# Kernel optimization log

Measured on AMD Instinct MI355X. Metric: run time of the kernel, lower is better.

Reference implementation:

```python
import jax, jax.numpy as jnp
import numpy as np
import math

B, S, D, H, F = 2, 2048, 1024, 16, 4096
DK = D // H
NEG_INF = -1000000000.0
EPS = 1e-5


def _layernorm(x, gamma, beta):
    # Faithful to source: torch.std default is unbiased (ddof=1), eps added to std
    mn = jnp.mean(x, axis=-1, keepdims=True)
    sd = jnp.std(x, axis=-1, keepdims=True, ddof=1)
    return (x - mn) / (sd + EPS) * gamma + beta


def _mha(xq, xkv, wq, bq, wk, bk, wv, bv, wo, bo, causal):
    b, sq, d = xq.shape
    sk = xkv.shape[1]
    q = (xq @ wq + bq).reshape(b, sq, H, DK).transpose(0, 2, 1, 3)   # [B,H,Sq,DK]
    k = (xkv @ wk + bk).reshape(b, sk, H, DK).transpose(0, 2, 1, 3)
    v = (xkv @ wv + bv).reshape(b, sk, H, DK).transpose(0, 2, 1, 3)
    scores = jnp.einsum('bhqd,bhkd->bhqk', q, k) / math.sqrt(DK)
    if causal:
        mask = jnp.triu(jnp.ones((sq, sk), dtype=scores.dtype), 1) * NEG_INF
        scores = scores + mask
    w = jax.nn.softmax(scores, axis=-1)
    att = jnp.einsum('bhqk,bhkd->bhqd', w, v).transpose(0, 2, 1, 3).reshape(b, sq, d)
    return att @ wo + bo


def setup_inputs() -> dict:
    key = jax.random.key(0)
    ks = jax.random.split(key, 32)
    it = iter(range(32))

    def lin(din, dout):
        kw = ks[next(it)]
        w = jax.random.normal(kw, (din, dout), jnp.float32) / math.sqrt(din)
        b = jnp.zeros((dout,), jnp.float32)
        return w, b

    X = jax.random.normal(ks[next(it)], (B, S, D), jnp.float32)
    y = jax.random.normal(ks[next(it)], (B, S, D), jnp.float32)
    wq1, bq1 = lin(D, D); wk1, bk1 = lin(D, D); wv1, bv1 = lin(D, D); wo1, bo1 = lin(D, D)
    wq2, bq2 = lin(D, D); wk2, bk2 = lin(D, D); wv2, bv2 = lin(D, D); wo2, bo2 = lin(D, D)
    wf1, bf1 = lin(D, F); wf2, bf2 = lin(F, D)
    g1 = jnp.ones((D,), jnp.float32); be1 = jnp.zeros((D,), jnp.float32)
    g2 = jnp.ones((D,), jnp.float32); be2 = jnp.zeros((D,), jnp.float32)
    g3 = jnp.ones((D,), jnp.float32); be3 = jnp.zeros((D,), jnp.float32)
    return dict(X=X, y=y,
                wq1=wq1, bq1=bq1, wk1=wk1, bk1=bk1, wv1=wv1, bv1=bv1, wo1=wo1, bo1=bo1,
                wq2=wq2, bq2=bq2, wk2=wk2, bk2=bk2, wv2=wv2, bv2=bv2, wo2=wo2, bo2=bo2,
                wf1=wf1, bf1=bf1, wf2=wf2, bf2=bf2,
                g1=g1, be1=be1, g2=g2, be2=be2, g3=g3, be3=be3)


def reference(X, y,
              wq1, bq1, wk1, bk1, wv1, bv1, wo1, bo1,
              wq2, bq2, wk2, bk2, wv2, bv2, wo2, bo2,
              wf1, bf1, wf2, bf2,
              g1, be1, g2, be2, g3, be3):
    # masked self-attention on decoder stream y (dropout = identity at inference)
    res = y
    out = _mha(y, y, wq1, bq1, wk1, bk1, wv1, bv1, wo1, bo1, causal=True)
    out = _layernorm(out + res, g1, be1)
    # cross-attention: queries from decoder, keys/values from encoder X
    res = out
    out = _mha(out, X, wq2, bq2, wk2, bk2, wv2, bv2, wo2, bo2, causal=False)
    out = _layernorm(out + res, g2, be2)
    # feed-forward (ReLU per intended semantics of the source)
    res = out
    out = jax.nn.relu(out @ wf1 + bf1) @ wf2 + bf2
    out = _layernorm(out + res, g3, be3)
    return out
```

## Files before the change

### kernel.cpp

```cpp
#include <hip/hip_runtime.h>

#define DEV __device__ __forceinline__

typedef __attribute__((ext_vector_type(8))) short short8;
typedef __attribute__((ext_vector_type(4))) float f32x4;
typedef __attribute__((ext_vector_type(4))) unsigned u32x4;

DEV unsigned short f2b(float f){
  unsigned r;
  asm("v_cvt_pk_bf16_f32 %0, %1, %1" : "=v"(r) : "v"(f));
  return (unsigned short)r;
}
DEV unsigned cvt_pk2(float lo, float hi){
  unsigned r;
  asm("v_cvt_pk_bf16_f32 %0, %1, %2" : "=v"(r) : "v"(lo), "v"(hi));
  return r;
}
DEV float b2f(unsigned short u){ unsigned v = ((unsigned)u)<<16; float f; __builtin_memcpy(&f,&v,4); return f; }

DEV void gload_lds16(const void* g, void* l){
  __builtin_amdgcn_global_load_lds((const __attribute__((address_space(1))) void*)g,
                                   (__attribute__((address_space(3))) void*)l, 16, 0, 0);
}

#define SCL 0.18033688011112042f

__global__ __launch_bounds__(256) void cvt_f32_bf16(
    const float* __restrict__ in, unsigned short* __restrict__ out, int n)
{
  int i = (blockIdx.x*256 + threadIdx.x)*4;
  if (i >= n) return;
  float4 v = *(const float4*)(in + i);
  uint2 o;
  o.x = cvt_pk2(v.x, v.y);
  o.y = cvt_pk2(v.z, v.w);
  *(uint2*)(out + i) = o;
}

struct TransAll {
  const float* W[10]; unsigned short* Wt[10];
  int K[10], N[10], swapxy[10];
};
__global__ __launch_bounds__(256) void transpose_cvt_all(TransAll p)
{
  const int z = blockIdx.z;
  const int bx = p.swapxy[z] ? blockIdx.y : blockIdx.x;
  const int by = p.swapxy[z] ? blockIdx.x : blockIdx.y;
  const int K = p.K[z], N = p.N[z];
  const int n0 = bx*32, k0 = by*32;
  if (n0 >= N || k0 >= K) return;
  const float* __restrict__ W = p.W[z];
  unsigned short* __restrict__ Wt = p.Wt[z];
  __shared__ float tile[32][33];
  int tx = threadIdx.x & 31, ty = threadIdx.x >> 5;
  #pragma unroll
  for (int j=0;j<32;j+=8)
    tile[ty+j][tx] = W[(size_t)(k0+ty+j)*N + n0+tx];
  __syncthreads();
  #pragma unroll
  for (int j=0;j<32;j+=8)
    Wt[(size_t)(n0+ty+j)*K + k0+tx] = f2b(tile[tx][ty+j]);
}

template<int EPI>
__global__ __launch_bounds__(256) void gemm_bt(
    const unsigned short* __restrict__ A,
    const unsigned short* __restrict__ Bt,
    const float* __restrict__ bias,
    unsigned short* __restrict__ C,
    int M, int N, int Kc, int LDA, int LDB)
{
  __shared__ alignas(16) unsigned short Asm_[128*32];
  __shared__ alignas(16) unsigned short Bsm_[128*32];
  const int tid = threadIdx.x;
  const int wave = tid>>6, lane = tid&63;
  const int r0 = lane&15, kq = (lane>>4)*8, cq = lane>>4;
  const int m0 = blockIdx.y*128, n0 = blockIdx.x*128;
  const int wr = wave>>1, wc = wave&1;
  const int koff = blockIdx.z * Kc;
  const bool addb = (blockIdx.z == 0);
  C += (size_t)blockIdx.z * M * N;

  f32x4 zero4 = {0.f,0.f,0.f,0.f};
  f32x4 acc[4][4];
  #pragma unroll
  for (int m=0;m<4;m++)
    #pragma unroll
    for (int n=0;n<4;n++) acc[m][n]=zero4;

  const int nk = Kc>>5;
  for (int kt=0; kt<nk; kt++){
    #pragma unroll
    for (int i=0;i<2;i++){
      int idx = i*256 + tid;
      int row = idx>>2, kc = (idx&3)<<3;
      gload_lds16(A  + (size_t)(m0+row)*LDA + koff + (kt<<5) + kc,
                  Asm_ + (size_t)(i*256 + wave*64)*8);
      gload_lds16(Bt + (size_t)(n0+row)*LDB + koff + (kt<<5) + kc,
                  Bsm_ + (size_t)(i*256 + wave*64)*8);
    }
    __syncthreads();
    short8 a[4], b[4];
    #pragma unroll
    for (int m=0;m<4;m++) a[m] = *(const short8*)&Asm_[(wr*64 + m*16 + r0)*32 + kq];
    #pragma unroll
    for (int n=0;n<4;n++) b[n] = *(const short8*)&Bsm_[(wc*64 + n*16 + r0)*32 + kq];
    #pragma unroll
    for (int m=0;m<4;m++)
      #pragma unroll
      for (int n=0;n<4;n++)
        acc[m][n] = __builtin_amdgcn_mfma_f32_16x16x32_bf16(a[m], b[n], acc[m][n], 0,0,0);
    __syncthreads();
  }

  #pragma unroll
  for (int n=0;n<4;n++){
    int col = n0 + wc*64 + n*16 + r0;
    float bs = addb ? bias[col] : 0.f;
    #pragma unroll
    for (int m=0;m<4;m++){
      int rowb = m0 + wr*64 + m*16 + cq*4;
      #pragma unroll
      for (int reg=0;reg<4;reg++){
        float v = acc[m][n][reg] + bs;
        if (EPI==1) v = fmaxf(v, 0.f);
        C[(size_t)(rowb+reg)*N + col] = f2b(v);
      }
    }
  }
}

struct QKVArgs { const unsigned short* Aw[3]; const float* bias[3]; unsigned short* out[3]; };
__global__ __launch_bounds__(256) void gemm_qkv(
    const unsigned short* __restrict__ Bt,
    QKVArgs args, int M, int K)
{
  __shared__ alignas(16) unsigned short Asm_[128*32];
  __shared__ alignas(16) unsigned short Bsm_[128*32];
  const int tid = threadIdx.x;
  const int wave = tid>>6, lane = tid&63;
  const int r0 = lane&15, kq = (lane>>4)*8, cq = lane>>4;
  const int m0 = blockIdx.y*128, n0 = blockIdx.x*128;
  const int wr = wave>>1, wc = wave&1;
  const int which = n0>>10;
  const unsigned short* __restrict__ A = args.Aw[which];

  f32x4 zero4 = {0.f,0.f,0.f,0.f};
  f32x4 acc[4][4];
  #pragma unroll
  for (int m=0;m<4;m++)
    #pragma unroll
    for (int n=0;n<4;n++) acc[m][n]=zero4;

  const int nk = K>>5;
  for (int kt=0; kt<nk; kt++){
    #pragma unroll
    for (int i=0;i<2;i++){
      int idx = i*256 + tid;
      int row = idx>>2, kc = (idx&3)<<3;
      gload_lds16(A  + (size_t)(m0+row)*K + (kt<<5) + kc,
                  Asm_ + (size_t)(i*256 + wave*64)*8);
      gload_lds16(Bt + (size_t)(n0+row)*K + (kt<<5) + kc,
                  Bsm_ + (size_t)(i*256 + wave*64)*8);
    }
    __syncthreads();
    short8 a[4], b[4];
    #pragma unroll
    for (int m=0;m<4;m++) a[m] = *(const short8*)&Asm_[(wr*64 + m*16 + r0)*32 + kq];
    #pragma unroll
    for (int n=0;n<4;n++) b[n] = *(const short8*)&Bsm_[(wc*64 + n*16 + r0)*32 + kq];
    #pragma unroll
    for (int m=0;m<4;m++)
      #pragma unroll
      for (int n=0;n<4;n++)
        acc[m][n] = __builtin_amdgcn_mfma_f32_16x16x32_bf16(a[m], b[n], acc[m][n], 0,0,0);
    __syncthreads();
  }

  const int n0l = n0 & 1023;
  unsigned short* __restrict__ Cout = args.out[which];
  const float* __restrict__ bp = args.bias[which];
  const bool isV = (which == 2);
  const float scl = (which == 0) ? SCL : 1.f;

  #pragma unroll
  for (int n=0;n<4;n++){
    int col = n0l + wc*64 + n*16 + r0;
    float bs = bp[col];
    int h_ = col>>6, dk = col&63;
    #pragma unroll
    for (int m=0;m<4;m++){
      int rowb = m0 + wr*64 + m*16 + cq*4;
      #pragma unroll
      for (int reg=0;reg<4;reg++){
        float v = (acc[m][n][reg] + bs) * scl;
        int row = rowb + reg;
        int b_ = row>>11, s_ = row&2047;
        if (isV){
          int sp = (s_ & ~31) | (((s_>>2)&3)<<3) | (((s_>>4)&1)<<2) | (s_&3);
          Cout[(((size_t)(b_*16+h_))*64 + dk)*2048 + sp] = f2b(v);
        } else {
          Cout[(((size_t)(b_*16+h_))*2048 + s_)*64 + dk] = f2b(v);
        }
      }
    }
  }
}

template<int MODE>
__global__ __launch_bounds__(256, 4) void attn_kernel(
    const unsigned short* __restrict__ Q,
    const unsigned short* __restrict__ K,
    const unsigned short* __restrict__ Vt,
    unsigned short* __restrict__ O,
    float* __restrict__ po, float* __restrict__ ml)
{
  __shared__ alignas(16) unsigned short Ksm[2][64*64];
  __shared__ alignas(16) unsigned short Vsm[2][64*64];
  const int S = 2048, DK = 64;
  const int h = blockIdx.y, b = blockIdx.z;
  const int tid = threadIdx.x, wave = tid>>6, lane = tid&63;
  const int r0 = lane&15, kq = (lane>>4)*8, cq = lane>>4;

  int qb, t0, t1, chunk = 0;
  bool partial = false;
  if (MODE==1){
    int bx = blockIdx.x;
    if (bx < 32){ qb = bx; t0 = 0; t1 = (qb<15?qb:15); chunk = 0; partial = (qb>=16); }
    else        { qb = bx-16; t0 = 16; t1 = qb; chunk = 1; partial = true; }
  } else { qb = blockIdx.x; t0 = 0; t1 = S/64 - 1; }

  const unsigned short* qh = Q  + ((size_t)(b*16+h))*S*DK;
  const unsigned short* kh = K  + ((size_t)(b*16+h))*S*DK;
  const unsigned short* vh = Vt + ((size_t)(b*16+h))*DK*S;

  const int idx0 = tid, idx1 = 256 + tid;
  const int row0 = idx0>>3, row1 = idx1>>3;
  const int cb0 = ((idx0&7) ^ (row0&7))<<3;
  const int cb1 = ((idx1&7) ^ (row1&7))<<3;
  const unsigned short* kg0 = kh + (size_t)row0*64 + cb0;
  const unsigned short* kg1 = kh + (size_t)row1*64 + cb1;
  const unsigned short* vg0 = vh + (size_t)row0*2048 + cb0;
  const unsigned short* vg1 = vh + (size_t)row1*2048 + cb1;
  const int l0 = wave*512, l1 = 2048 + wave*512;
  const int swr = (r0&7)<<3;

  short8 qa[2];
  {
    int qrow = qb*64 + wave*16 + r0;
    qa[0] = *(const short8*)&qh[(size_t)qrow*DK + kq];
    qa[1] = *(const short8*)&qh[(size_t)qrow*DK + 32 + kq];
  }
  short8 vones;
  #pragma unroll
  for (int j=0;j<8;j++) vones[j] = (short)0x3F80;

  f32x4 zero4 = {0.f,0.f,0.f,0.f};
  f32x4 o[4];
  float lr = 0.f;
  #pragma unroll
  for (int n=0;n<4;n++) o[n]=zero4;

  gload_lds16(kg0 + (size_t)t0*4096, &Ksm[0][l0]);
  gload_lds16(kg1 + (size_t)t0*4096, &Ksm[0][l1]);
  gload_lds16(vg0 + (size_t)t0*64,   &Vsm[0][l0]);
  gload_lds16(vg1 + (size_t)t0*64,   &Vsm[0][l1]);
  __syncthreads();

  int cur = 0;
  for (int t=t0; t<=t1; t++){
    if (t < t1){
      gload_lds16(kg0 + (size_t)(t+1)*4096, &Ksm[cur^1][l0]);
      gload_lds16(kg1 + (size_t)(t+1)*4096, &Ksm[cur^1][l1]);
      gload_lds16(vg0 + (size_t)(t+1)*64,   &Vsm[cur^1][l0]);
      gload_lds16(vg1 + (size_t)(t+1)*64,   &Vsm[cur^1][l1]);
    }

    f32x4 sv[4];
    #pragma unroll
    for (int n=0;n<4;n++) sv[n]=zero4;
    #pragma unroll
    for (int n=0;n<4;n++)
      #pragma unroll
      for (int kk=0;kk<2;kk++){
        short8 kb = *(const short8*)&Ksm[cur][(((n*16 + r0)*64) + kk*32 + kq) ^ swr];
        sv[n] = __builtin_amdgcn_mfma_f32_16x16x32_bf16(kb, qa[kk], sv[n], 0,0,0);
      }
    if (MODE==1 && t==qb){
      const int qg = wave*16 + r0;
      #pragma unroll
      for (int n=0;n<4;n++)
        #pragma unroll
        for (int reg=0;reg<4;reg++){
          if (n*16 + cq*4 + reg > qg) sv[n][reg] += -1000000000.0f;
        }
    }

    #pragma unroll
    for (int n=0;n<4;n++)
      #pragma unroll
      for (int reg=0;reg<4;reg++)
        sv[n][reg] = exp2f(sv[n][reg]);

    short8 pa[2];
    #pragma unroll
    for (int kk=0;kk<2;kk++){
      u32x4 w;
      w[0] = cvt_pk2(sv[2*kk][0],   sv[2*kk][1]);
      w[1] = cvt_pk2(sv[2*kk][2],   sv[2*kk][3]);
      w[2] = cvt_pk2(sv[2*kk+1][0], sv[2*kk+1][1]);
      w[3] = cvt_pk2(sv[2*kk+1][2], sv[2*kk+1][3]);
      pa[kk] = __builtin_bit_cast(short8, w);
    }

    {
      f32x4 ls = zero4;
      ls = __builtin_amdgcn_mfma_f32_16x16x32_bf16(vones, pa[0], ls, 0,0,0);
      ls = __builtin_amdgcn_mfma_f32_16x16x32_bf16(vones, pa[1], ls, 0,0,0);
      lr += ls[0];
    }

    #pragma unroll
    for (int n=0;n<4;n++)
      #pragma unroll
      for (int kk=0;kk<2;kk++){
        short8 vb = *(const short8*)&Vsm[cur][(((n*16 + r0)*64) + kk*32 + cq*8) ^ swr];
        o[n] = __builtin_amdgcn_mfma_f32_16x16x32_bf16(vb, pa[kk], o[n], 0,0,0);
      }

    __syncthreads();
    cur ^= 1;
  }

  if (MODE==1 && partial){
    float* pop = po + (size_t)chunk*2097152;
    float* mlp = ml + (size_t)chunk*32768;
    const int bh = b*16 + h, qb16 = qb - 16;
    const int rowIdx = (bh*16 + qb16)*64 + wave*16 + r0;
    if (cq == 0) mlp[rowIdx] = lr;
    #pragma unroll
    for (int n=0;n<4;n++){
      float4 v; v.x=o[n][0]; v.y=o[n][1]; v.z=o[n][2]; v.w=o[n][3];
      *(float4*)&pop[(size_t)rowIdx*64 + n*16 + cq*4] = v;
    }
  } else {
    const int sg = qb*64 + wave*16 + r0;
    const float inv = 1.f / lr;
    unsigned short* op = O + ((size_t)b*S + sg)*1024 + h*64;
    #pragma unroll
    for (int n=0;n<4;n++){
      uint2 w;
      w.x = cvt_pk2(o[n][0]*inv, o[n][1]*inv);
      w.y = cvt_pk2(o[n][2]*inv, o[n][3]*inv);
      *(uint2*)(op + n*16 + cq*4) = w;
    }
  }
}

__global__ __launch_bounds__(256) void attn_merge(
    const float* __restrict__ po, const float* __restrict__ ml,
    unsigned short* __restrict__ O)
{
  int gid = blockIdx.x*256 + threadIdx.x;
  int row = gid>>4, dq = (gid&15)*4;
  float l0 = ml[row], l1 = ml[32768 + row];
  float inv = 1.f / (l0 + l1);
  float4 v0 = *(const float4*)(po + (size_t)row*64 + dq);
  float4 v1 = *(const float4*)(po + 2097152 + (size_t)row*64 + dq);
  float r0 = (v0.x + v1.x)*inv;
  float r1 = (v0.y + v1.y)*inv;
  float r2 = (v0.z + v1.z)*inv;
  float r3 = (v0.w + v1.w)*inv;
  int bh = row>>10, qb16 = (row>>6)&15, qr = row&63;
  int b = bh>>4, h = bh&15;
  int s = (16+qb16)*64 + qr;
  unsigned short* op = O + ((size_t)b*2048 + s)*1024 + h*64 + dq;
  uint2 out; out.x = cvt_pk2(r0, r1); out.y = cvt_pk2(r2, r3);
  *(uint2*)op = out;
}

template<int OUT_F32>
__global__ __launch_bounds__(256) void add_ln3(
    const unsigned short* __restrict__ a0, const unsigned short* __restrict__ a1,
    const unsigned short* __restrict__ r,
    const float* __restrict__ g, const float* __restrict__ be, void* outp)
{
  const int row = blockIdx.x, tid = threadIdx.x;
  const size_t base = (size_t)row*1024 + tid*4;
  ushort4 va = *(const ushort4*)(a0 + base);
  ushort4 vb_ = *(const ushort4*)(a1 + base);
  ushort4 vr = *(const ushort4*)(r + base);
  float x[4];
  x[0] = b2f(va.x)+b2f(vb_.x)+b2f(vr.x);
  x[1] = b2f(va.y)+b2f(vb_.y)+b2f(vr.y);
  x[2] = b2f(va.z)+b2f(vb_.z)+b2f(vr.z);
  x[3] = b2f(va.w)+b2f(vb_.w)+b2f(vr.w);
  float s = x[0]+x[1]+x[2]+x[3];
  float ss = x[0]*x[0]+x[1]*x[1]+x[2]*x[2]+x[3]*x[3];
  #pragma unroll
  for (int d=1;d<64;d<<=1){ s += __shfl_xor(s,d,64); ss += __shfl_xor(ss,d,64); }
  __shared__ float rs[4], rss[4];
  int wave = tid>>6, lane = tid&63;
  if (lane==0){ rs[wave]=s; rss[wave]=ss; }
  __syncthreads();
  s = rs[0]+rs[1]+rs[2]+rs[3];
  ss = rss[0]+rss[1]+rss[2]+rss[3];
  float mean = s*(1.f/1024.f);
  float var = (ss - 1024.f*mean*mean)*(1.f/1023.f);
  float sd = sqrtf(fmaxf(var,0.f));
  float inv = 1.f/(sd + 1e-5f);
  float4 vg = *(const float4*)(g + tid*4);
  float4 vbe = *(const float4*)(be + tid*4);
  float o0 = (x[0]-mean)*inv*vg.x+vbe.x;
  float o1 = (x[1]-mean)*inv*vg.y+vbe.y;
  float o2 = (x[2]-mean)*inv*vg.z+vbe.z;
  float o3 = (x[3]-mean)*inv*vg.w+vbe.w;
  if (OUT_F32){
    float4 vo; vo.x=o0; vo.y=o1; vo.z=o2; vo.w=o3;
    *(float4*)((float*)outp + base) = vo;
  } else {
    uint2 vo; vo.x = cvt_pk2(o0,o1); vo.y = cvt_pk2(o2,o3);
    *(uint2*)((unsigned short*)outp + base) = vo;
  }
}

extern "C" void kernel_launch(void* const* d_in, const int* in_sizes, int n_in,
                              void* d_out, int out_size, void* d_ws, size_t ws_size,
                              hipStream_t stream)
{
  typedef const float* cf;
  cf X   = (cf)d_in[0],  y   = (cf)d_in[1];
  cf wq1 = (cf)d_in[2],  bq1 = (cf)d_in[3],  wk1 = (cf)d_in[4],  bk1 = (cf)d_in[5];
  cf wv1 = (cf)d_in[6],  bv1 = (cf)d_in[7],  wo1 = (cf)d_in[8],  bo1 = (cf)d_in[9];
  cf wq2 = (cf)d_in[10], bq2 = (cf)d_in[11], wk2 = (cf)d_in[12], bk2 = (cf)d_in[13];
  cf wv2 = (cf)d_in[14], bv2 = (cf)d_in[15], wo2 = (cf)d_in[16], bo2 = (cf)d_in[17];
  cf wf1 = (cf)d_in[18], bf1 = (cf)d_in[19], wf2 = (cf)d_in[20], bf2 = (cf)d_in[21];
  cf g1  = (cf)d_in[22], be1 = (cf)d_in[23], g2  = (cf)d_in[24], be2 = (cf)d_in[25];
  cf g3  = (cf)d_in[26], be3 = (cf)d_in[27];

  char* ws = (char*)d_ws;
  const size_t MB = 1u<<20;
  unsigned short* wq1t = (unsigned short*)(ws + 0*MB);
  unsigned short* wk1t = (unsigned short*)(ws + 2*MB);
  unsigned short* wv1t = (unsigned short*)(ws + 4*MB);
  unsigned short* wo1t = (unsigned short*)(ws + 6*MB);
  unsigned short* wq2t = (unsigned short*)(ws + 8*MB);
  unsigned short* wk2t = (unsigned short*)(ws + 10*MB);
  unsigned short* wv2t = (unsigned short*)(ws + 12*MB);
  unsigned short* wo2t = (unsigned short*)(ws + 14*MB);
  unsigned short* wf1t = (unsigned short*)(ws + 16*MB);
  unsigned short* wf2t = (unsigned short*)(ws + 24*MB);
  unsigned short* Qb   = (unsigned short*)(ws + 32*MB);
  unsigned short* Kb   = (unsigned short*)(ws + 40*MB);
  unsigned short* Vtb  = (unsigned short*)(ws + 48*MB);
  unsigned short* attno= (unsigned short*)(ws + 56*MB);
  unsigned short* hbuf = (unsigned short*)(ws + 32*MB);
  unsigned short* part = (unsigned short*)(ws + 64*MB);
  float*          poF  = (float*)(ws + 64*MB);
  float*          mlF  = (float*)(ws + 80*MB);
  unsigned short* x1b  = (unsigned short*)(ws + 80*MB);
  unsigned short* slot = (unsigned short*)(ws + 88*MB);
  unsigned short* yb = slot, *Xb = slot, *x2b = slot;

  dim3 blk(256);
  const int NTOK = 2*2048*1024;
  cvt_f32_bf16<<<NTOK/1024, blk, 0, stream>>>(y, yb, NTOK);

  {
    TransAll tp;
    const float* Ws[10]   = {wq1,wk1,wv1,wo1,wq2,wk2,wv2,wo2,wf1,wf2};
    unsigned short* Ts[10]= {wq1t,wk1t,wv1t,wo1t,wq2t,wk2t,wv2t,wo2t,wf1t,wf2t};
    for (int i=0;i<10;i++){
      tp.W[i]=Ws[i]; tp.Wt[i]=Ts[i];
      tp.K[i] = (i==9)?4096:1024;
      tp.N[i] = (i==8)?4096:1024;
      tp.swapxy[i] = (i==9)?1:0;
    }
    transpose_cvt_all<<<dim3(128,32,10), blk, 0, stream>>>(tp);
  }

  dim3 gqkv(24,32);
  dim3 gs(8,32,2);
  dim3 gff1(32,32,1);
  dim3 gac(48,16,2);
  dim3 gax(32,16,2);

  {
    QKVArgs a1;
    a1.Aw[0]=yb; a1.Aw[1]=yb; a1.Aw[2]=yb;
    a1.bias[0]=bq1; a1.bias[1]=bk1; a1.bias[2]=bv1;
    a1.out[0]=Qb; a1.out[1]=Kb; a1.out[2]=Vtb;
    gemm_qkv<<<gqkv, blk, 0, stream>>>(wq1t, a1, 4096, 1024);
  }
  attn_kernel<1><<<gac, blk, 0, stream>>>(Qb, Kb, Vtb, attno, poF, mlF);
  attn_merge<<<2048, blk, 0, stream>>>(poF, mlF, attno);
  gemm_bt<0><<<gs, blk, 0, stream>>>(attno, wo1t, bo1, part, 4096, 1024, 512, 1024, 1024);
  add_ln3<0><<<4096, blk, 0, stream>>>(part, part+4194304, yb, g1, be1, x1b);

  cvt_f32_bf16<<<NTOK/1024, blk, 0, stream>>>(X, Xb, NTOK);
  {
    QKVArgs a2;
    a2.Aw[0]=x1b; a2.Aw[1]=Xb; a2.Aw[2]=Xb;
    a2.bias[0]=bq2; a2.bias[1]=bk2; a2.bias[2]=bv2;
    a2.out[0]=Qb; a2.out[1]=Kb; a2.out[2]=Vtb;
    gemm_qkv<<<gqkv, blk, 0, stream>>>(wq2t, a2, 4096, 1024);
  }
  attn_kernel<0><<<gax, blk, 0, stream>>>(Qb, Kb, Vtb, attno, nullptr, nullptr);
  gemm_bt<0><<<gs, blk, 0, stream>>>(attno, wo2t, bo2, part, 4096, 1024, 512, 1024, 1024);
  add_ln3<0><<<4096, blk, 0, stream>>>(part, part+4194304, x1b, g2, be2, x2b);

  gemm_bt<1><<<gff1, blk, 0, stream>>>(x2b, wf1t, bf1, hbuf, 4096, 4096, 1024, 1024, 1024);
  gemm_bt<0><<<gs, blk, 0, stream>>>(hbuf, wf2t, bf2, part, 4096, 1024, 2048, 4096, 4096);
  add_ln3<1><<<4096, blk, 0, stream>>>(part, part+4194304, x2b, g3, be3, d_out);
}
```

Before: 413.2 us.

## Split cross-attention over key halves and pipeline K/V loads with waitcnt barriers

Cross-attention now runs in a new mode that splits the key range into two halves. Each half writes unnormalized bf16 partial outputs and row sums, which a new merge kernel adds and normalizes. Separately, the per-tile __syncthreads calls become explicit s_waitcnt vmcnt plus s_barrier, so the prefetch of the next K/V tile can stay in flight while the current tile is computed. The split doubles the block count for finer scheduling, but it adds an extra launch, partial-buffer traffic and bf16 rounding of the partials.

```diff
diff --git a/kernel.cpp b/kernel.cpp
--- a/kernel.cpp
+++ b/kernel.cpp
@@ -213,7 +213,8 @@
     const unsigned short* __restrict__ K,
     const unsigned short* __restrict__ Vt,
     unsigned short* __restrict__ O,
-    float* __restrict__ po, float* __restrict__ ml)
+    float* __restrict__ po, unsigned short* __restrict__ pob,
+    float* __restrict__ ml)
 {
   __shared__ alignas(16) unsigned short Ksm[2][64*64];
   __shared__ alignas(16) unsigned short Vsm[2][64*64];
@@ -228,7 +229,12 @@
     int bx = blockIdx.x;
     if (bx < 32){ qb = bx; t0 = 0; t1 = (qb<15?qb:15); chunk = 0; partial = (qb>=16); }
     else        { qb = bx-16; t0 = 16; t1 = qb; chunk = 1; partial = true; }
-  } else { qb = blockIdx.x; t0 = 0; t1 = S/64 - 1; }
+  } else {
+    int bx = blockIdx.x;
+    if (bx < 32){ qb = bx; t0 = 0; t1 = 15; chunk = 0; }
+    else        { qb = bx-32; t0 = 16; t1 = 31; chunk = 1; }
+    partial = true;
+  }
 
   const unsigned short* qh = Q  + ((size_t)(b*16+h))*S*DK;
   const unsigned short* kh = K  + ((size_t)(b*16+h))*S*DK;
@@ -265,7 +271,6 @@
   gload_lds16(kg1 + (size_t)t0*4096, &Ksm[0][l1]);
   gload_lds16(vg0 + (size_t)t0*64,   &Vsm[0][l0]);
   gload_lds16(vg1 + (size_t)t0*64,   &Vsm[0][l1]);
-  __syncthreads();
 
   int cur = 0;
   for (int t=t0; t<=t1; t++){
@@ -274,7 +279,12 @@
       gload_lds16(kg1 + (size_t)(t+1)*4096, &Ksm[cur^1][l1]);
       gload_lds16(vg0 + (size_t)(t+1)*64,   &Vsm[cur^1][l0]);
       gload_lds16(vg1 + (size_t)(t+1)*64,   &Vsm[cur^1][l1]);
-    }
+      asm volatile("s_waitcnt vmcnt(4)" ::: "memory");
+    } else {
+      asm volatile("s_waitcnt vmcnt(0)" ::: "memory");
+    }
+    __builtin_amdgcn_s_barrier();
+    asm volatile("" ::: "memory");
 
     f32x4 sv[4];
     #pragma unroll
@@ -328,7 +338,9 @@
         o[n] = __builtin_amdgcn_mfma_f32_16x16x32_bf16(vb, pa[kk], o[n], 0,0,0);
       }
 
-    __syncthreads();
+    asm volatile("" ::: "memory");
+    __builtin_amdgcn_s_barrier();
+    asm volatile("" ::: "memory");
     cur ^= 1;
   }
 
@@ -342,6 +354,19 @@
     for (int n=0;n<4;n++){
       float4 v; v.x=o[n][0]; v.y=o[n][1]; v.z=o[n][2]; v.w=o[n][3];
       *(float4*)&pop[(size_t)rowIdx*64 + n*16 + cq*4] = v;
+    }
+  } else if (MODE==2){
+    unsigned short* pop = pob + (size_t)chunk*4194304;
+    float* mlp = ml + (size_t)chunk*65536;
+    const int bh = b*16 + h;
+    const int rowIdx = (bh*32 + qb)*64 + wave*16 + r0;
+    if (cq == 0) mlp[rowIdx] = lr;
+    #pragma unroll
+    for (int n=0;n<4;n++){
+      uint2 w;
+      w.x = cvt_pk2(o[n][0], o[n][1]);
+      w.y = cvt_pk2(o[n][2], o[n][3]);
+      *(uint2*)(pop + (size_t)rowIdx*64 + n*16 + cq*4) = w;
     }
   } else {
     const int sg = qb*64 + wave*16 + r0;
@@ -374,6 +399,27 @@
   int bh = row>>10, qb16 = (row>>6)&15, qr = row&63;
   int b = bh>>4, h = bh&15;
   int s = (16+qb16)*64 + qr;
+  unsigned short* op = O + ((size_t)b*2048 + s)*1024 + h*64 + dq;
+  uint2 out; out.x = cvt_pk2(r0, r1); out.y = cvt_pk2(r2, r3);
+  *(uint2*)op = out;
+}
+
+__global__ __launch_bounds__(256) void attn_merge_x(
+    const unsigned short* __restrict__ pob, const float* __restrict__ ml,
+    unsigned short* __restrict__ O)
+{
+  int gid = blockIdx.x*256 + threadIdx.x;
+  int row = gid>>4, dq = (gid&15)*4;
+  float l0 = ml[row], l1 = ml[65536 + row];
+  float inv = 1.f / (l0 + l1);
+  ushort4 u0 = *(const ushort4*)(pob + (size_t)row*64 + dq);
+  ushort4 u1 = *(const ushort4*)(pob + 4194304 + (size_t)row*64 + dq);
+  float r0 = (b2f(u0.x) + b2f(u1.x))*inv;
+  float r1 = (b2f(u0.y) + b2f(u1.y))*inv;
+  float r2 = (b2f(u0.z) + b2f(u1.z))*inv;
+  float r3 = (b2f(u0.w) + b2f(u1.w))*inv;
+  int bh = row>>11, s = row&2047;
+  int b = bh>>4, h = bh&15;
   unsigned short* op = O + ((size_t)b*2048 + s)*1024 + h*64 + dq;
   uint2 out; out.x = cvt_pk2(r0, r1); out.y = cvt_pk2(r2, r3);
   *(uint2*)op = out;
@@ -457,10 +503,12 @@
   unsigned short* hbuf = (unsigned short*)(ws + 32*MB);
   unsigned short* part = (unsigned short*)(ws + 64*MB);
   float*          poF  = (float*)(ws + 64*MB);
+  unsigned short* pobF = (unsigned short*)(ws + 64*MB);
   float*          mlF  = (float*)(ws + 80*MB);
   unsigned short* x1b  = (unsigned short*)(ws + 80*MB);
   unsigned short* slot = (unsigned short*)(ws + 88*MB);
   unsigned short* yb = slot, *Xb = slot, *x2b = slot;
+  float*          mlX  = (float*)(ws + 88*MB);
 
   dim3 blk(256);
   const int NTOK = 2*2048*1024;
@@ -483,7 +531,7 @@
   dim3 gs(8,32,2);
   dim3 gff1(32,32,1);
   dim3 gac(48,16,2);
-  dim3 gax(32,16,2);
+  dim3 gax(64,16,2);
 
   {
     QKVArgs a1;
@@ -492,7 +540,7 @@
     a1.out[0]=Qb; a1.out[1]=Kb; a1.out[2]=Vtb;
     gemm_qkv<<<gqkv, blk, 0, stream>>>(wq1t, a1, 4096, 1024);
   }
-  attn_kernel<1><<<gac, blk, 0, stream>>>(Qb, Kb, Vtb, attno, poF, mlF);
+  attn_kernel<1><<<gac, blk, 0, stream>>>(Qb, Kb, Vtb, attno, poF, nullptr, mlF);
   attn_merge<<<2048, blk, 0, stream>>>(poF, mlF, attno);
   gemm_bt<0><<<gs, blk, 0, stream>>>(attno, wo1t, bo1, part, 4096, 1024, 512, 1024, 1024);
   add_ln3<0><<<4096, blk, 0, stream>>>(part, part+4194304, yb, g1, be1, x1b);
@@ -505,7 +553,8 @@
     a2.out[0]=Qb; a2.out[1]=Kb; a2.out[2]=Vtb;
     gemm_qkv<<<gqkv, blk, 0, stream>>>(wq2t, a2, 4096, 1024);
   }
-  attn_kernel<0><<<gax, blk, 0, stream>>>(Qb, Kb, Vtb, attno, nullptr, nullptr);
+  attn_kernel<2><<<gax, blk, 0, stream>>>(Qb, Kb, Vtb, attno, nullptr, pobF, mlX);
+  attn_merge_x<<<4096, blk, 0, stream>>>(pobF, mlX, attno);
   gemm_bt<0><<<gs, blk, 0, stream>>>(attno, wo2t, bo2, part, 4096, 1024, 512, 1024, 1024);
   add_ln3<0><<<4096, blk, 0, stream>>>(part, part+4194304, x1b, g2, be2, x2b);
 
```

After: 415.3 us. About the same (+0.5%).
